# Performance work log

Hardware: AMD Instinct MI355X
Metric: run time of the kernel (lower is better)

The kernel has to match this reference:

```python
import jax, jax.numpy as jnp
from jax import lax
import numpy as np

EPS = 1e-5

def _conv1x1(x, w, b=None):
    # x: [B,C,H,W], w: [O,C]
    y = jnp.einsum('oc,bchw->bohw', w, x)
    if b is not None:
        y = y + b[:, None, None]
    return y

def _bn(x, g, b, m, v):
    scale = g / jnp.sqrt(v + EPS)
    return (x - m[:, None, None]) * scale[:, None, None] + b[:, None, None]

def _conv_bn_silu(x, w, g, b, m, v):
    return jax.nn.silu(_bn(_conv1x1(x, w), g, b, m, v))

def _maxpool(x, k):
    p = k // 2
    return lax.reduce_window(x, -jnp.inf, lax.max, (1, 1, k, k), (1, 1, 1, 1),
                             ((0, 0), (0, 0), (p, p), (p, p)))

def _avgpool(x, k):
    # torch AvgPool2d default count_include_pad=True -> divide by k*k
    p = k // 2
    s = lax.reduce_window(x, 0.0, lax.add, (1, 1, k, k), (1, 1, 1, 1),
                          ((0, 0), (0, 0), (p, p), (p, p)))
    return s / float(k * k)

def setup_inputs() -> dict:
    key = jax.random.key(0)
    ks = jax.random.split(key, 18)
    f32 = jnp.float32
    B, C1, H, W = 8, 512, 64, 64
    c_ = C1 // 2          # 256
    C = c_ * 7            # 1792
    Cq = C // 8           # 224
    C2 = 512
    rn = lambda i, sh, s: jax.random.normal(ks[i], sh, dtype=f32) * s
    return {
        'x': rn(0, (B, C1, H, W), 1.0),
        'cv1_w': rn(1, (c_, C1), 0.05),
        'cv1_g': jax.random.uniform(ks[2], (c_,), dtype=f32),
        'cv1_b': rn(3, (c_,), 0.05),
        'cv1_m': jnp.zeros((c_,), f32),
        'cv1_v': jnp.ones((c_,), f32),
        'q_w': rn(4, (Cq, C), 0.02),
        'q_b': rn(5, (Cq,), 0.02),
        'k_w': rn(6, (Cq, C), 0.02),
        'k_b': rn(7, (Cq,), 0.02),
        'v_w': rn(8, (C, C), 0.02),
        'v_b': rn(9, (C,), 0.02),
        'gamma': rn(10, (1,), 0.5),
        'cv2_w': rn(11, (C2, C), 0.02),
        'cv2_g': jax.random.uniform(ks[12], (C2,), dtype=f32),
        'cv2_b': rn(13, (C2,), 0.05),
        'cv2_m': jnp.zeros((C2,), f32),
        'cv2_v': jnp.ones((C2,), f32),
    }

def _criss_cross(cat, q_w, q_b, k_w, k_b, v_w, v_b, gamma):
    B, C, H, W = cat.shape
    q = _conv1x1(cat, q_w, q_b)   # [B,Cq,H,W]
    k = _conv1x1(cat, k_w, k_b)
    v = _conv1x1(cat, v_w, v_b)   # [B,C,H,W]
    # column (H-axis) energies with -inf diagonal, row (W-axis) energies
    eH = jnp.einsum('bchw,bcgw->bhwg', q, k)        # [B,H,W,H]
    diag = jnp.eye(H, dtype=bool)[:, None, :]       # mask where h == g
    eH = jnp.where(diag, -jnp.inf, eH)
    eW = jnp.einsum('bchw,bchv->bhwv', q, k)        # [B,H,W,W]
    att = jax.nn.softmax(jnp.concatenate([eH, eW], axis=-1), axis=-1)
    attH, attW = att[..., :H], att[..., H:]
    outH = jnp.einsum('bcgw,bhwg->bchw', v, attH)
    outW = jnp.einsum('bchv,bhwv->bchw', v, attW)
    return gamma[0] * (outH + outW) + cat

def reference(x, cv1_w, cv1_g, cv1_b, cv1_m, cv1_v,
              q_w, q_b, k_w, k_b, v_w, v_b, gamma,
              cv2_w, cv2_g, cv2_b, cv2_m, cv2_v):
    x1 = _conv_bn_silu(x, cv1_w, cv1_g, cv1_b, cv1_m, cv1_v)   # [B,256,H,W]
    y1 = _maxpool(x1, 5)
    y2 = _maxpool(y1, 5)
    y3 = _maxpool(y2, 5)
    a1 = _avgpool(x1, 13)
    a2 = _avgpool(x1, 9)
    a3 = _avgpool(x1, 5)
    cat = jnp.concatenate([x1, y1, y2, y3, a1, a2, a3], axis=1)  # [B,1792,H,W]
    att = _criss_cross(cat, q_w, q_b, k_w, k_b, v_w, v_b, gamma)
    return _conv_bn_silu(att, cv2_w, cv2_g, cv2_b, cv2_m, cv2_v)
```

## Files before the change

### kernel.cpp

```cpp
#include <hip/hip_runtime.h>


typedef short bf16x8 __attribute__((ext_vector_type(8)));
typedef float f32x4  __attribute__((ext_vector_type(4)));

#define DEV __device__ __forceinline__

DEV float bf2f(unsigned short u) {
    unsigned int i = ((unsigned int)u) << 16;
    float f; __builtin_memcpy(&f, &i, 4); return f;
}
DEV unsigned short f2bf(float f) {
    unsigned int i; __builtin_memcpy(&i, &f, 4);
    unsigned int r = i + 0x7FFFu + ((i >> 16) & 1u);
    return (unsigned short)(r >> 16);
}
DEV float fsilu(float v) { return v / (1.f + __expf(-v)); }

#define GLL(gsrc, ldst)                                                        \
    __builtin_amdgcn_global_load_lds(                                          \
        (const __attribute__((address_space(1))) unsigned int*)(gsrc),         \
        (__attribute__((address_space(3))) unsigned int*)(ldst), 16, 0, 0)

#define MFMA(a, b, c) __builtin_amdgcn_mfma_f32_16x16x32_bf16((a), (b), (c), 0, 0, 0)

#define SBAR do {                                                              \
    __builtin_amdgcn_sched_barrier(0);                                         \
    __builtin_amdgcn_s_barrier();                                              \
    __builtin_amdgcn_sched_barrier(0); } while (0)
#define LGKM0 do {                                                             \
    asm volatile("s_waitcnt lgkmcnt(0)" ::: "memory");                         \
    __builtin_amdgcn_sched_barrier(0); } while (0)
#define VMC(n) do {                                                            \
    asm volatile("s_waitcnt vmcnt(" #n ")" ::: "memory");                      \
    __builtin_amdgcn_sched_barrier(0); } while (0)

__global__ __launch_bounds__(256) void prep_kernel(
    const float* __restrict__ cv1_w, const float* __restrict__ cv1_g,
    const float* __restrict__ cv1_b, const float* __restrict__ cv1_m,
    const float* __restrict__ cv1_v,
    const float* __restrict__ q_w, const float* __restrict__ q_b,
    const float* __restrict__ k_w, const float* __restrict__ k_b,
    const float* __restrict__ v_b, const float* __restrict__ gamma,
    const float* __restrict__ cv2_w, const float* __restrict__ cv2_g,
    const float* __restrict__ cv2_b, const float* __restrict__ cv2_m,
    const float* __restrict__ cv2_v,
    unsigned short* __restrict__ wb1, unsigned short* __restrict__ wqk,
    unsigned short* __restrict__ wc2,
    float* __restrict__ sc1, float* __restrict__ sh1,
    float* __restrict__ sc2, float* __restrict__ sh2,
    float* __restrict__ qkb, float* __restrict__ zeros)
{
    for (int i = blockIdx.x * 256 + threadIdx.x; i < 917504;
         i += gridDim.x * 256) {
        wc2[i] = f2bf(cv2_w[i]);
        int row = i / 1792;
        int col = i - row * 1792;
        float qv = (row < 224) ? q_w[i]
                   : (row < 448) ? k_w[(row - 224) * 1792 + col] : 0.f;
        wqk[i] = f2bf(qv);
        if (i < 131072) wb1[i] = f2bf(cv1_w[i]);
        if (i < 1792) zeros[i] = 0.f;
        if (i < 512) {
            qkb[i] = (i < 224) ? q_b[i] : (i < 448 ? k_b[i - 224] : 0.f);
            float sc = cv2_g[i] * rsqrtf(cv2_v[i] + 1e-5f);
            float dot = 0.f;
            for (int k = 0; k < 1792; ++k) dot += cv2_w[i * 1792 + k] * v_b[k];
            sc2[i] = sc;
            sh2[i] = cv2_b[i] - cv2_m[i] * sc + sc * gamma[0] * dot;
        }
        if (i < 256) {
            float sc = cv1_g[i] * rsqrtf(cv1_v[i] + 1e-5f);
            sc1[i] = sc; sh1[i] = cv1_b[i] - cv1_m[i] * sc;
        }
    }
}

__global__ __launch_bounds__(256) void transpose_x(
    const float* __restrict__ x, unsigned short* __restrict__ xT)
{
    int bid = blockIdx.x;
    int nt = bid & 63, ct = (bid >> 6) & 7, b = bid >> 9;
    __shared__ float tile[64][65];
    int tid = threadIdx.x;
    int n0 = nt * 64, c0 = ct * 64;
#pragma unroll
    for (int it = 0; it < 16; ++it) {
        int idx = tid + it * 256;
        int r = idx >> 6, cc = idx & 63;
        tile[r][cc] = x[((long)(b * 512 + c0 + r)) * 4096 + n0 + cc];
    }
    __syncthreads();
#pragma unroll
    for (int it = 0; it < 16; ++it) {
        int idx = tid + it * 256;
        int r = idx >> 6, cc = idx & 63;
        xT[((long)(b * 4096 + n0 + r)) * 512 + c0 + cc] = f2bf(tile[cc][r]);
    }
}

__global__ __launch_bounds__(256) void transpose_w(
    const float* __restrict__ w, unsigned short* __restrict__ wT)
{
    int bid = blockIdx.x;
    int tx = bid % 28, ty = bid / 28;
    __shared__ float tile[64][65];
    int tid = threadIdx.x;
#pragma unroll
    for (int it = 0; it < 16; ++it) {
        int idx = tid + it * 256;
        int r = idx >> 6, cc = idx & 63;
        tile[r][cc] = w[((long)(ty * 64 + r)) * 1792 + tx * 64 + cc];
    }
    __syncthreads();
#pragma unroll
    for (int it = 0; it < 16; ++it) {
        int idx = tid + it * 256;
        int r = idx >> 6, cc = idx & 63;
        wT[((long)(tx * 64 + r)) * 1792 + ty * 64 + cc] = f2bf(tile[cc][r]);
    }
}

template <int EPI, bool DUAL>
__global__ __launch_bounds__(512, 2) void gemm256(
    const unsigned short* __restrict__ A, const unsigned short* __restrict__ B,
    const unsigned short* __restrict__ A2, const unsigned short* __restrict__ B2,
    int lda, int ldb, int K1, int K2,
    void* __restrict__ outp, int ldo,
    const float* __restrict__ p0, const float* __restrict__ p1)
{
    __shared__ __align__(16) unsigned short Ash[2][2][8192];
    __shared__ __align__(16) unsigned short Bsh[2][2][8192];
    const int tid = threadIdx.x, lane = tid & 63, wave = tid >> 6;
    const int wm = wave >> 2, wn = wave & 3;
    const long tile_m = (long)blockIdx.x * 256;
    const long tile_n = (long)blockIdx.y * 256;
    const int r0 = tid >> 2;
    const int ke0 = ((tid & 3) * 8) ^ (16 * ((r0 >> 3) & 1));
    const unsigned short* As0 = A + (tile_m + r0) * (long)lda + ke0;
    const unsigned short* As1 = A + (tile_m + r0 + 128) * (long)lda + ke0;
    const unsigned short* Bs0 = B + (tile_n + r0) * (long)ldb + ke0;
    const unsigned short* Bs1 = B + (tile_n + r0 + 128) * (long)ldb + ke0;
    const unsigned short* Cs0 = DUAL ? A2 + (tile_m + r0) * (long)lda + ke0 : As0;
    const unsigned short* Cs1 = DUAL ? A2 + (tile_m + r0 + 128) * (long)lda + ke0 : As1;
    const unsigned short* Ds0 = DUAL ? B2 + (tile_n + r0) * (long)ldb + ke0 : Bs0;
    const unsigned short* Ds1 = DUAL ? B2 + (tile_n + r0 + 128) * (long)ldb + ke0 : Bs1;
    const int dst0 = wave * 512;
    const int dst1 = 4096 + wave * 512;
    const int arow = lane & 15;
    const int kgs = ((lane >> 4) << 3) ^ (16 * ((arow >> 3) & 1));
    f32x4 acc[8][4] = {};
    bf16x8 a[8], b[4];
    const int nt1 = K1 >> 6;
    const int nt = nt1 + (DUAL ? (K2 >> 6) : 0);

#define PA0(t) ((DUAL && (t) >= nt1) ? Cs0 + (long)((t) - nt1) * 64 : As0 + (long)(t) * 64)
#define PA1(t) ((DUAL && (t) >= nt1) ? Cs1 + (long)((t) - nt1) * 64 : As1 + (long)(t) * 64)
#define PB0(t) ((DUAL && (t) >= nt1) ? Ds0 + (long)((t) - nt1) * 64 : Bs0 + (long)(t) * 64)
#define PB1(t) ((DUAL && (t) >= nt1) ? Ds1 + (long)((t) - nt1) * 64 : Bs1 + (long)(t) * 64)
#define STGA(db, kh, t) do {                                                   \
    GLL(PA0(t) + (kh) * 32, &Ash[db][kh][dst0]);                               \
    GLL(PA1(t) + (kh) * 32, &Ash[db][kh][dst1]); } while (0)
#define STGB(db, kh, t) do {                                                   \
    GLL(PB0(t) + (kh) * 32, &Bsh[db][kh][dst0]);                               \
    GLL(PB1(t) + (kh) * 32, &Bsh[db][kh][dst1]); } while (0)
#define LDA8(db, ks) do { _Pragma("unroll")                                    \
    for (int m = 0; m < 8; ++m)                                                \
        a[m] = *(const bf16x8*)&Ash[db][ks][(wm * 128 + m * 16 + arow) * 32 + kgs]; \
    } while (0)
#define LDB1(db, ks, n, slot)                                                  \
    b[slot] = *(const bf16x8*)&Bsh[db][ks][(wn * 64 + (n) * 16 + arow) * 32 + kgs]
#define MMA2(lo) do {                                                          \
    __builtin_amdgcn_s_setprio(1);                                             \
    _Pragma("unroll")                                                          \
    for (int m = 0; m < 8; ++m) {                                              \
        acc[m][lo]     = MFMA(a[m], b[lo],     acc[m][lo]);                    \
        acc[m][lo + 1] = MFMA(a[m], b[lo + 1], acc[m][lo + 1]);                \
    }                                                                          \
    __builtin_amdgcn_s_setprio(0); } while (0)

    STGA(0, 0, 0); STGB(0, 0, 0); STGA(0, 1, 0); STGB(0, 1, 0);
    VMC(4);
    SBAR;

    for (int kt = 0; kt < nt; ++kt) {
        const int db = kt & 1, sb = db ^ 1;
        const bool stg = (kt + 1 < nt);
        const int kn = kt + 1;
        LDA8(db, 0);
        LDB1(db, 0, 0, 0); LDB1(db, 0, 1, 1);
        if (stg) STGA(sb, 0, kn);
        SBAR; LGKM0;
        MMA2(0);
        SBAR;
        LDB1(db, 0, 2, 2); LDB1(db, 0, 3, 3);
        if (stg) STGB(sb, 0, kn);
        SBAR; LGKM0;
        MMA2(2);
        if (kt + 1 < nt) { VMC(4); } else { VMC(0); }
        SBAR;
        LDA8(db, 1);
        LDB1(db, 1, 0, 0); LDB1(db, 1, 1, 1);
        if (stg) STGA(sb, 1, kn);
        SBAR; LGKM0;
        MMA2(0);
        SBAR;
        LDB1(db, 1, 2, 2); LDB1(db, 1, 3, 3);
        if (stg) STGB(sb, 1, kn);
        SBAR; LGKM0;
        MMA2(2);
        if (stg) VMC(4);
        SBAR;
    }

    const int rbase = (lane >> 4) << 2;
#pragma unroll
    for (int n = 0; n < 4; ++n) {
        const int gcol = (int)tile_n + wn * 64 + n * 16 + arow;
        const float s0 = p0[gcol];
        const float s1 = (EPI != 1) ? p1[gcol] : 0.f;
#pragma unroll
        for (int m = 0; m < 8; ++m) {
            const long grow0 = tile_m + wm * 128 + m * 16 + rbase;
            if (EPI == 4) {
                const long bb = grow0 >> 12, pix = grow0 & 4095;
                float4 o4;
#pragma unroll
                for (int r = 0; r < 4; ++r) {
                    float v = acc[m][n][r] * s0 + s1;
                    ((float*)&o4)[r] = fsilu(v);
                }
                *(float4*)&((float*)outp)[((bb * 512 + gcol)) * 4096 + pix] = o4;
            } else {
#pragma unroll
                for (int r = 0; r < 4; ++r) {
                    float v = acc[m][n][r];
                    if (EPI != 1) { v = v * s0 + s1; v = fsilu(v); }
                    else          { v += s0; }
                    ((unsigned short*)outp)[(grow0 + r) * ldo + gcol] = f2bf(v);
                }
            }
        }
    }
#undef PA0
#undef PA1
#undef PB0
#undef PB1
#undef STGA
#undef STGB
#undef LDA8
#undef LDB1
#undef MMA2
}

__global__ __launch_bounds__(256) void pool_h(
    const unsigned short* __restrict__ catT, unsigned short* __restrict__ pool)
{
    const int b = blockIdx.x >> 6, h = blockIdx.x & 63;
    __shared__ __align__(16) unsigned short x1s[64 * 256];
    __shared__ __align__(16) unsigned short rm5[64 * 256];
    const int tid = threadIdx.x, lane = tid & 63, wave = tid >> 6;
    const long nb = (long)b * 4096 + h * 64;
#pragma unroll
    for (int j = 0; j < 8; ++j) {
        int o = wave * 8192 + j * 1024 + lane * 16;
        int w = o >> 9, c = (o & 511) >> 1;
        GLL(catT + (nb + w) * 1792 + c,
            (char*)x1s + (wave * 8192 + j * 1024));
    }
    __syncthreads();
    const int c = tid;
    for (int w = 0; w < 64; ++w) {
        int lo = (w >= 2) ? w - 2 : 0, hi = (w <= 61) ? w + 2 : 63;
        float m = bf2f(x1s[lo * 256 + c]);
        for (int d = lo + 1; d <= hi; ++d) m = fmaxf(m, bf2f(x1s[d * 256 + c]));
        rm5[w * 256 + c] = f2bf(m);
    }
    float s5 = 0.f, s9 = 0.f, s13 = 0.f;
#pragma unroll
    for (int d = 0; d <= 2; ++d) s5  += bf2f(x1s[d * 256 + c]);
#pragma unroll
    for (int d = 0; d <= 4; ++d) s9  += bf2f(x1s[d * 256 + c]);
#pragma unroll
    for (int d = 0; d <= 6; ++d) s13 += bf2f(x1s[d * 256 + c]);
    unsigned short* q0 = pool;
    unsigned short* q1 = pool + (long)32768 * 256;
    unsigned short* q2 = pool + (long)32768 * 512;
    unsigned short* q3 = pool + (long)32768 * 768;
    unsigned short* q4 = pool + (long)32768 * 1024;
    unsigned short* q5 = pool + (long)32768 * 1280;
    const long wb = (long)b * 4096 + h;
    for (int w = 0; w < 64; ++w) {
        long off = (wb + (long)w * 64) * 256 + c;
        float v5 = bf2f(rm5[w * 256 + c]);
        int wm2 = (w >= 2) ? w - 2 : 0, wp2 = (w <= 61) ? w + 2 : 63;
        int wm4 = (w >= 4) ? w - 4 : 0, wp4 = (w <= 59) ? w + 4 : 63;
        float v9  = fmaxf(bf2f(rm5[wm2 * 256 + c]), bf2f(rm5[wp2 * 256 + c]));
        float v13 = fmaxf(v5, fmaxf(bf2f(rm5[wm4 * 256 + c]),
                                    bf2f(rm5[wp4 * 256 + c])));
        q0[off] = f2bf(v5);  q1[off] = f2bf(v9);  q2[off] = f2bf(v13);
        q3[off] = f2bf(s5);  q4[off] = f2bf(s9);  q5[off] = f2bf(s13);
        if (w + 3 <= 63) s5  += bf2f(x1s[(w + 3) * 256 + c]);
        if (w - 2 >= 0)  s5  -= bf2f(x1s[(w - 2) * 256 + c]);
        if (w + 5 <= 63) s9  += bf2f(x1s[(w + 5) * 256 + c]);
        if (w - 4 >= 0)  s9  -= bf2f(x1s[(w - 4) * 256 + c]);
        if (w + 7 <= 63) s13 += bf2f(x1s[(w + 7) * 256 + c]);
        if (w - 6 >= 0)  s13 -= bf2f(x1s[(w - 6) * 256 + c]);
    }
}

template <int I>
__global__ __launch_bounds__(256) void pool_v(
    const unsigned short* __restrict__ pool, unsigned short* __restrict__ catT)
{
    constexpr int R = 2 * (I + 1);
    constexpr int K = 2 * R + 1;
    constexpr float SCL = (I == 0) ? (1.f / 25.f)
                        : (I == 1) ? (1.f / 81.f) : (1.f / 169.f);
    constexpr int MAXD = 256 * (I + 1);
    constexpr int SUMD = 1536 - 256 * I;
    const int bid = blockIdx.x;
    const int chh = bid & 1, w = (bid >> 1) & 63, b = bid >> 7;
    const int c0 = chh * 128;
    __shared__ __align__(16) unsigned short mslab[64 * 128];
    __shared__ __align__(16) unsigned short sslab[64 * 128];
    const int tid = threadIdx.x, lane = tid & 63, wave = tid >> 6;
    const long sbase = ((long)b * 4096 + (long)w * 64) * 256 + c0;
    const unsigned short* msrc = pool + (long)I * 32768 * 256 + sbase;
    const unsigned short* ssrc = pool + (long)(I + 3) * 32768 * 256 + sbase;
#pragma unroll
    for (int j = 0; j < 4; ++j) {
        int o = j * 4096 + wave * 1024 + lane * 16;
        int hh = o >> 8, ce = (o & 255) >> 1;
        GLL(msrc + hh * 256 + ce, (char*)mslab + (j * 4096 + wave * 1024));
        GLL(ssrc + hh * 256 + ce, (char*)sslab + (j * 4096 + wave * 1024));
    }
    __syncthreads();
    const int c = tid & 127, hg = tid >> 7;
    const int h0 = hg * 32;
    const long dbase = ((long)b * 4096 + w) * 1792 + c0 + c;
    float pre[32];
    {
        float run = -1e30f;
        int ph = (h0 + 2 * R - (K - 1)) % K;
#pragma unroll
        for (int t = 0; t < 32 + K - 1; ++t) {
            int p = h0 + R - (K - 1) + t;
            if (ph == 0) run = -1e30f;
            float v = ((unsigned)p < 64u) ? bf2f(mslab[p * 128 + c]) : -1e30f;
            run = fmaxf(run, v);
            if (t >= K - 1) pre[t - (K - 1)] = run;
            ph = (ph + 1 == K) ? 0 : ph + 1;
        }
    }
    {
        float run = -1e30f;
        int ph = (h0 + 31 + (K - 1)) % K;
#pragma unroll
        for (int t = 0; t < 32 + K - 1; ++t) {
            int s = h0 + 31 - R + (K - 1) - t;
            if (ph == K - 1) run = -1e30f;
            float v = ((unsigned)s < 64u) ? bf2f(mslab[s * 128 + c]) : -1e30f;
            run = fmaxf(run, v);
            if (t >= K - 1) {
                int h = s + R;
                catT[dbase + MAXD + (long)h * (64 * 1792)] =
                    f2bf(fmaxf(run, pre[31 + (K - 1) - t]));
            }
            ph = (ph == 0) ? K - 1 : ph - 1;
        }
    }
    {
        float s = 0.f;
        int lo0 = (h0 - R >= 0) ? h0 - R : 0;
        int hi0 = (h0 + R <= 63) ? h0 + R : 63;
        for (int d = lo0; d <= hi0; ++d) s += bf2f(sslab[d * 128 + c]);
        for (int hh = 0; hh < 32; ++hh) {
            int h = h0 + hh;
            catT[dbase + SUMD + (long)h * (64 * 1792)] = f2bf(s * SCL);
            if (h + 1 + R <= 63) s += bf2f(sslab[(h + 1 + R) * 128 + c]);
            if (h - R >= 0)      s -= bf2f(sslab[(h - R) * 128 + c]);
        }
    }
}

__global__ __launch_bounds__(256) void scores_h(
    const unsigned short* __restrict__ qk, float* __restrict__ attHlog)
{
    const int b = blockIdx.x >> 6, w = blockIdx.x & 63;
    __shared__ __align__(16) unsigned short Qs[64 * 232];
    __shared__ __align__(16) unsigned short Ks[64 * 232];
    const int tid = threadIdx.x, lane = tid & 63, wave = tid >> 6;
#pragma unroll
    for (int j = 0; j < 14; ++j) {
        int idx = tid + j * 256;
        int s = idx >= 1792;
        int id2 = idx - s * 1792;
        int row = id2 / 28, cb = id2 - row * 28;
        bf16x8 v = *(const bf16x8*)(qk + ((long)b * 4096 + row * 64 + w) * 512 +
                                    s * 224 + cb * 8);
        *(bf16x8*)((s ? Ks : Qs) + row * 232 + cb * 8) = v;
    }
    __syncthreads();
    const int m0 = wave * 16, arow = lane & 15, kc = (lane >> 4) << 3;
    f32x4 acc[4] = {};
#pragma unroll
    for (int ks = 0; ks < 7; ++ks) {
        bf16x8 af = *(const bf16x8*)(Qs + (m0 + arow) * 232 + ks * 32 + kc);
#pragma unroll
        for (int nf = 0; nf < 4; ++nf) {
            bf16x8 bv = *(const bf16x8*)(Ks + (nf * 16 + arow) * 232 + ks * 32 + kc);
            acc[nf] = MFMA(af, bv, acc[nf]);
        }
    }
    const int rb = (lane >> 4) << 2;
#pragma unroll
    for (int nf = 0; nf < 4; ++nf) {
        int g = nf * 16 + arow;
#pragma unroll
        for (int r = 0; r < 4; ++r) {
            int h = m0 + rb + r;
            float v = acc[nf][r];
            if (g == h) v = -1e30f;
            attHlog[((long)(b * 64 + h) * 64 + w) * 64 + g] = v;
        }
    }
}

__global__ __launch_bounds__(256) void scores_w_softmax(
    const unsigned short* __restrict__ qk, const float* __restrict__ attHlog,
    unsigned short* __restrict__ att)
{
    const int b = blockIdx.x >> 6, h = blockIdx.x & 63;
    __shared__ __align__(16) unsigned short Qs[64 * 232];
    __shared__ __align__(16) unsigned short Ks[64 * 232];
    __shared__ float ews[64 * 65];
    const int tid = threadIdx.x, lane = tid & 63, wave = tid >> 6;
    const long nbase = (long)b * 4096 + h * 64;
#pragma unroll
    for (int j = 0; j < 14; ++j) {
        int idx = tid + j * 256;
        int s = idx >= 1792;
        int id2 = idx - s * 1792;
        int row = id2 / 28, cb = id2 - row * 28;
        bf16x8 v = *(const bf16x8*)(qk + (nbase + row) * 512 + s * 224 + cb * 8);
        *(bf16x8*)((s ? Ks : Qs) + row * 232 + cb * 8) = v;
    }
    __syncthreads();
    const int m0 = wave * 16, arow = lane & 15, kc = (lane >> 4) << 3;
    f32x4 acc[4] = {};
#pragma unroll
    for (int ks = 0; ks < 7; ++ks) {
        bf16x8 af = *(const bf16x8*)(Qs + (m0 + arow) * 232 + ks * 32 + kc);
#pragma unroll
        for (int nf = 0; nf < 4; ++nf) {
            bf16x8 bv = *(const bf16x8*)(Ks + (nf * 16 + arow) * 232 + ks * 32 + kc);
            acc[nf] = MFMA(af, bv, acc[nf]);
        }
    }
    const int rb = (lane >> 4) << 2;
#pragma unroll
    for (int nf = 0; nf < 4; ++nf)
#pragma unroll
        for (int r = 0; r < 4; ++r)
            ews[(m0 + rb + r) * 65 + nf * 16 + arow] = acc[nf][r];
    __syncthreads();
    const int wl = tid >> 2, p = tid & 3;
    float eh[16], ew[16];
    const float* hrow = attHlog + ((long)(b * 64 + h) * 64 + wl) * 64 + p * 16;
#pragma unroll
    for (int j = 0; j < 16; ++j) eh[j] = hrow[j];
#pragma unroll
    for (int j = 0; j < 16; ++j) ew[j] = ews[wl * 65 + p * 16 + j];
    float mx = -1e30f;
#pragma unroll
    for (int j = 0; j < 16; ++j) { mx = fmaxf(mx, eh[j]); mx = fmaxf(mx, ew[j]); }
    mx = fmaxf(mx, __shfl_xor(mx, 1));
    mx = fmaxf(mx, __shfl_xor(mx, 2));
    float sm = 0.f;
#pragma unroll
    for (int j = 0; j < 16; ++j) {
        eh[j] = __expf(eh[j] - mx); sm += eh[j];
        ew[j] = __expf(ew[j] - mx); sm += ew[j];
    }
    sm += __shfl_xor(sm, 1);
    sm += __shfl_xor(sm, 2);
    float inv = 1.f / sm;
    unsigned short* orow = att + ((long)(b * 64 + h) * 64 + wl) * 128;
#pragma unroll
    for (int j = 0; j < 16; ++j) orow[p * 16 + j] = f2bf(eh[j] * inv);
#pragma unroll
    for (int j = 0; j < 16; ++j) orow[64 + p * 16 + j] = f2bf(ew[j] * inv);
}

template <int MODE>
__global__ __launch_bounds__(256) void apply_att(
    const unsigned short* __restrict__ att, const unsigned short* __restrict__ vsrc,
    unsigned short* __restrict__ mixed, const float* __restrict__ gamma)
{
    const int ch = blockIdx.x & 3;
    const int i  = (blockIdx.x >> 2) & 63;
    const int b  = blockIdx.x >> 8;
    const int c0 = ch * 448;
    __shared__ __align__(16) unsigned short As[64 * 72];
    __shared__ __align__(16) unsigned short Vs[64 * 448];
    const int tid = threadIdx.x, lane = tid & 63, wave = tid >> 6;
#pragma unroll
    for (int j = 0; j < 2; ++j) {
        int idx = tid + j * 256;
        int hh = idx >> 3, cb = idx & 7;
        long pos = (MODE == 0) ? ((long)(b * 64 + hh) * 64 + i)
                               : ((long)(b * 64 + i) * 64 + hh);
        bf16x8 v = *(const bf16x8*)(att + pos * 128 + MODE * 64 + cb * 8);
        *(bf16x8*)(As + hh * 72 + cb * 8) = v;
    }
#pragma unroll
    for (int j = 0; j < 14; ++j) {
        int idx = tid + j * 256;
        int g = idx / 56, cb = idx - g * 56;
        long n = (MODE == 0) ? ((long)b * 4096 + g * 64 + i)
                             : ((long)b * 4096 + i * 64 + g);
        bf16x8 v = *(const bf16x8*)(vsrc + n * 1792 + c0 + cb * 8);
        int sw = (g >> 3) & 7;
        *(bf16x8*)(Vs + g * 448 + ((cb ^ sw) << 3)) = v;
    }
    __syncthreads();
    const int arow = lane & 15, kc8 = (lane >> 4) << 3;
    const int rb = (lane >> 4) << 2;
    f32x4 acc[4][7] = {};
#pragma unroll
    for (int ks = 0; ks < 2; ++ks) {
        const int k0 = ks * 32;
        bf16x8 af[4];
#pragma unroll
        for (int m = 0; m < 4; ++m)
            af[m] = *(const bf16x8*)(As + (m * 16 + arow) * 72 + k0 + kc8);
        const int g0 = k0 + kc8;
        const int sw = (g0 >> 3) & 7;
#pragma unroll
        for (int nf = 0; nf < 7; ++nf) {
            int cl = wave * 112 + nf * 16 + arow;
            int cb = cl >> 3, clo = cl & 7;
            const unsigned short* pp = Vs + g0 * 448 + ((cb ^ sw) << 3) + clo;
            bf16x8 bv;
#pragma unroll
            for (int j = 0; j < 8; ++j) bv[j] = (short)pp[j * 448];
#pragma unroll
            for (int m = 0; m < 4; ++m)
                acc[m][nf] = MFMA(af[m], bv, acc[m][nf]);
        }
    }
    const float gam = gamma[0];
#pragma unroll
    for (int nf = 0; nf < 7; ++nf) {
        const int c = c0 + wave * 112 + nf * 16 + arow;
#pragma unroll
        for (int m = 0; m < 4; ++m) {
#pragma unroll
            for (int r = 0; r < 4; ++r) {
                const int rl = m * 16 + rb + r;
                long n = (MODE == 0) ? ((long)b * 4096 + rl * 64 + i)
                                     : ((long)b * 4096 + i * 64 + rl);
                long idx2 = n * 1792 + c;
                if (MODE == 0) {
                    mixed[idx2] = f2bf(acc[m][nf][r]);
                } else {
                    float pv = bf2f(mixed[idx2]);
                    mixed[idx2] = f2bf(gam * (acc[m][nf][r] + pv));
                }
            }
        }
    }
}

extern "C" void kernel_launch(void* const* d_in, const int* in_sizes, int n_in,
                              void* d_out, int out_size, void* d_ws, size_t ws_size,
                              hipStream_t stream)
{
    const float* x     = (const float*)d_in[0];
    const float* cv1_w = (const float*)d_in[1];
    const float* cv1_g = (const float*)d_in[2];
    const float* cv1_b = (const float*)d_in[3];
    const float* cv1_m = (const float*)d_in[4];
    const float* cv1_v = (const float*)d_in[5];
    const float* q_w   = (const float*)d_in[6];
    const float* q_b   = (const float*)d_in[7];
    const float* k_w   = (const float*)d_in[8];
    const float* k_b   = (const float*)d_in[9];
    const float* v_w   = (const float*)d_in[10];
    const float* v_b   = (const float*)d_in[11];
    const float* gamma = (const float*)d_in[12];
    const float* cv2_w = (const float*)d_in[13];
    const float* cv2_g = (const float*)d_in[14];
    const float* cv2_b = (const float*)d_in[15];
    const float* cv2_m = (const float*)d_in[16];
    const float* cv2_v = (const float*)d_in[17];

    char* ws = (char*)d_ws;
    unsigned short* wb1  = (unsigned short*)(ws + 0);
    unsigned short* wqk  = (unsigned short*)(ws + 262144);
    unsigned short* wc2  = (unsigned short*)(ws + 2097152);
    unsigned short* w2g  = (unsigned short*)(ws + 3932160);
    float* sc1           = (float*)(ws + 5767168);
    float* sh1           = (float*)(ws + 5775360);
    float* sc2           = (float*)(ws + 5783552);
    float* sh2           = (float*)(ws + 5791744);
    float* qkb           = (float*)(ws + 5799936);
    float* zeros         = (float*)(ws + 5808128);
    unsigned short* catT = (unsigned short*)(ws + 6291456);
    const long C_OFF = 123731968;
    unsigned short* xT    = (unsigned short*)(ws + C_OFF);
    unsigned short* wvT   = (unsigned short*)(ws + C_OFF + 33554432);
    unsigned short* poolb = (unsigned short*)(ws + C_OFF);
    unsigned short* mixed = (unsigned short*)(ws + C_OFF);
    unsigned short* qk    = (unsigned short*)d_out;
    float* attHlog        = (float*)((char*)d_out + 33554432);
    unsigned short* attb  = (unsigned short*)((char*)d_out + 41943040);

    prep_kernel<<<1024, 256, 0, stream>>>(
        cv1_w, cv1_g, cv1_b, cv1_m, cv1_v, q_w, q_b, k_w, k_b, v_b, gamma,
        cv2_w, cv2_g, cv2_b, cv2_m, cv2_v,
        wb1, wqk, wc2, sc1, sh1, sc2, sh2, qkb, zeros);

    transpose_x<<<4096, 256, 0, stream>>>(x, xT);
    transpose_w<<<784, 256, 0, stream>>>(v_w, wvT);

    gemm256<1, false><<<dim3(2, 7), 512, 0, stream>>>(
        wc2, wvT, wc2, wvT, 1792, 1792, 1792, 0, w2g, 1792, zeros, nullptr);

    gemm256<0, false><<<dim3(128, 1), 512, 0, stream>>>(
        xT, wb1, xT, wb1, 512, 512, 512, 0, catT, 1792, sc1, sh1);

    pool_h<<<512, 256, 0, stream>>>(catT, poolb);
    pool_v<0><<<1024, 256, 0, stream>>>(poolb, catT);
    pool_v<1><<<1024, 256, 0, stream>>>(poolb, catT);
    pool_v<2><<<1024, 256, 0, stream>>>(poolb, catT);

    gemm256<1, false><<<dim3(128, 2), 512, 0, stream>>>(
        catT, wqk, catT, wqk, 1792, 1792, 1792, 0, qk, 512, qkb, nullptr);

    scores_h<<<512, 256, 0, stream>>>(qk, attHlog);
    scores_w_softmax<<<512, 256, 0, stream>>>(qk, attHlog, attb);

    apply_att<0><<<2048, 256, 0, stream>>>(attb, catT, mixed, gamma);
    apply_att<1><<<2048, 256, 0, stream>>>(attb, catT, mixed, gamma);

    gemm256<4, true><<<dim3(128, 2), 512, 0, stream>>>(
        mixed, w2g, catT, wc2, 1792, 1792, 1792, 1792, d_out, 0, sc2, sh2);
}
```

Before: 640.1 us.

## Deepen GEMM LDS prefetch pipeline and split horizontal pooling per kernel size

```diff
diff --git a/kernel.cpp b/kernel.cpp
--- a/kernel.cpp
+++ b/kernel.cpp
@@ -179,37 +179,42 @@
     }                                                                          \
     __builtin_amdgcn_s_setprio(0); } while (0)
 
-    STGA(0, 0, 0); STGB(0, 0, 0); STGA(0, 1, 0); STGB(0, 1, 0);
-    VMC(4);
+    STGA(0, 0, 0); STGB(0, 0, 0);
+    STGA(0, 1, 0); STGB(0, 1, 0);
+    {
+        const int t1p = (1 < nt) ? 1 : 0;
+        STGA(1, 0, t1p); STGB(1, 0, t1p);
+    }
+    VMC(8);
     SBAR;
 
     for (int kt = 0; kt < nt; ++kt) {
         const int db = kt & 1, sb = db ^ 1;
-        const bool stg = (kt + 1 < nt);
-        const int kn = kt + 1;
+        const int t1c = (kt + 1 < nt) ? kt + 1 : nt - 1;
+        const int t2c = (kt + 2 < nt) ? kt + 2 : nt - 1;
         LDA8(db, 0);
         LDB1(db, 0, 0, 0); LDB1(db, 0, 1, 1);
-        if (stg) STGA(sb, 0, kn);
+        STGA(sb, 1, t1c);
         SBAR; LGKM0;
         MMA2(0);
         SBAR;
         LDB1(db, 0, 2, 2); LDB1(db, 0, 3, 3);
-        if (stg) STGB(sb, 0, kn);
+        STGB(sb, 1, t1c);
         SBAR; LGKM0;
         MMA2(2);
-        if (kt + 1 < nt) { VMC(4); } else { VMC(0); }
+        VMC(8);
         SBAR;
         LDA8(db, 1);
         LDB1(db, 1, 0, 0); LDB1(db, 1, 1, 1);
-        if (stg) STGA(sb, 1, kn);
+        STGA(db, 0, t2c);
         SBAR; LGKM0;
         MMA2(0);
         SBAR;
         LDB1(db, 1, 2, 2); LDB1(db, 1, 3, 3);
-        if (stg) STGB(sb, 1, kn);
+        STGB(db, 0, t2c);
         SBAR; LGKM0;
         MMA2(2);
-        if (stg) VMC(4);
+        VMC(8);
         SBAR;
     }
 
@@ -253,59 +258,71 @@
 #undef MMA2
 }
 
-__global__ __launch_bounds__(256) void pool_h(
+template <int I>
+__global__ __launch_bounds__(512) void pool_hk(
     const unsigned short* __restrict__ catT, unsigned short* __restrict__ pool)
 {
+    constexpr int R = 2 * (I + 1);
+    constexpr int K = 2 * R + 1;
     const int b = blockIdx.x >> 6, h = blockIdx.x & 63;
     __shared__ __align__(16) unsigned short x1s[64 * 256];
-    __shared__ __align__(16) unsigned short rm5[64 * 256];
     const int tid = threadIdx.x, lane = tid & 63, wave = tid >> 6;
     const long nb = (long)b * 4096 + h * 64;
 #pragma unroll
-    for (int j = 0; j < 8; ++j) {
-        int o = wave * 8192 + j * 1024 + lane * 16;
-        int w = o >> 9, c = (o & 511) >> 1;
-        GLL(catT + (nb + w) * 1792 + c,
-            (char*)x1s + (wave * 8192 + j * 1024));
-    }
-    __syncthreads();
-    const int c = tid;
-    for (int w = 0; w < 64; ++w) {
-        int lo = (w >= 2) ? w - 2 : 0, hi = (w <= 61) ? w + 2 : 63;
-        float m = bf2f(x1s[lo * 256 + c]);
-        for (int d = lo + 1; d <= hi; ++d) m = fmaxf(m, bf2f(x1s[d * 256 + c]));
-        rm5[w * 256 + c] = f2bf(m);
-    }
-    float s5 = 0.f, s9 = 0.f, s13 = 0.f;
-#pragma unroll
-    for (int d = 0; d <= 2; ++d) s5  += bf2f(x1s[d * 256 + c]);
-#pragma unroll
-    for (int d = 0; d <= 4; ++d) s9  += bf2f(x1s[d * 256 + c]);
-#pragma unroll
-    for (int d = 0; d <= 6; ++d) s13 += bf2f(x1s[d * 256 + c]);
-    unsigned short* q0 = pool;
-    unsigned short* q1 = pool + (long)32768 * 256;
-    unsigned short* q2 = pool + (long)32768 * 512;
-    unsigned short* q3 = pool + (long)32768 * 768;
-    unsigned short* q4 = pool + (long)32768 * 1024;
-    unsigned short* q5 = pool + (long)32768 * 1280;
-    const long wb = (long)b * 4096 + h;
-    for (int w = 0; w < 64; ++w) {
-        long off = (wb + (long)w * 64) * 256 + c;
-        float v5 = bf2f(rm5[w * 256 + c]);
-        int wm2 = (w >= 2) ? w - 2 : 0, wp2 = (w <= 61) ? w + 2 : 63;
-        int wm4 = (w >= 4) ? w - 4 : 0, wp4 = (w <= 59) ? w + 4 : 63;
-        float v9  = fmaxf(bf2f(rm5[wm2 * 256 + c]), bf2f(rm5[wp2 * 256 + c]));
-        float v13 = fmaxf(v5, fmaxf(bf2f(rm5[wm4 * 256 + c]),
-                                    bf2f(rm5[wp4 * 256 + c])));
-        q0[off] = f2bf(v5);  q1[off] = f2bf(v9);  q2[off] = f2bf(v13);
-        q3[off] = f2bf(s5);  q4[off] = f2bf(s9);  q5[off] = f2bf(s13);
-        if (w + 3 <= 63) s5  += bf2f(x1s[(w + 3) * 256 + c]);
-        if (w - 2 >= 0)  s5  -= bf2f(x1s[(w - 2) * 256 + c]);
-        if (w + 5 <= 63) s9  += bf2f(x1s[(w + 5) * 256 + c]);
-        if (w - 4 >= 0)  s9  -= bf2f(x1s[(w - 4) * 256 + c]);
-        if (w + 7 <= 63) s13 += bf2f(x1s[(w + 7) * 256 + c]);
-        if (w - 6 >= 0)  s13 -= bf2f(x1s[(w - 6) * 256 + c]);
+    for (int j = 0; j < 4; ++j) {
+        int chunk = j * 8 + wave;
+        int o = chunk * 1024 + lane * 16;
+        int e = o >> 1, w = e >> 8, c = e & 255;
+        GLL(catT + (nb + w) * 1792 + c, (char*)x1s + chunk * 1024);
+    }
+    __syncthreads();
+    const int c = tid & 255, wg = tid >> 8;
+    const int w0 = wg * 32;
+    unsigned short* qm = pool + (long)I * 32768 * 256;
+    unsigned short* qs = pool + (long)(I + 3) * 32768 * 256;
+    const long obase = ((long)b * 4096 + h) * 256 + c;
+    float pre[32];
+    {
+        float run = -1e30f;
+        int ph = (w0 + 2 * R - (K - 1)) % K;
+#pragma unroll
+        for (int t = 0; t < 32 + K - 1; ++t) {
+            int p = w0 + R - (K - 1) + t;
+            if (ph == 0) run = -1e30f;
+            float v = ((unsigned)p < 64u) ? bf2f(x1s[p * 256 + c]) : -1e30f;
+            run = fmaxf(run, v);
+            if (t >= K - 1) pre[t - (K - 1)] = run;
+            ph = (ph + 1 == K) ? 0 : ph + 1;
+        }
+    }
+    {
+        float run = -1e30f;
+        int ph = (w0 + 31 + (K - 1)) % K;
+#pragma unroll
+        for (int t = 0; t < 32 + K - 1; ++t) {
+            int s = w0 + 31 - R + (K - 1) - t;
+            if (ph == K - 1) run = -1e30f;
+            float v = ((unsigned)s < 64u) ? bf2f(x1s[s * 256 + c]) : -1e30f;
+            run = fmaxf(run, v);
+            if (t >= K - 1) {
+                int w = s + R;
+                qm[obase + (long)w * 16384] =
+                    f2bf(fmaxf(run, pre[31 + (K - 1) - t]));
+            }
+            ph = (ph == 0) ? K - 1 : ph - 1;
+        }
+    }
+    {
+        float s = 0.f;
+        int lo0 = (w0 - R >= 0) ? w0 - R : 0;
+        int hi0 = (w0 + R <= 63) ? w0 + R : 63;
+        for (int d = lo0; d <= hi0; ++d) s += bf2f(x1s[d * 256 + c]);
+        for (int ww = 0; ww < 32; ++ww) {
+            int w = w0 + ww;
+            qs[obase + (long)w * 16384] = f2bf(s);
+            if (w + 1 + R <= 63) s += bf2f(x1s[(w + 1 + R) * 256 + c]);
+            if (w - R >= 0)      s -= bf2f(x1s[(w - R) * 256 + c]);
+        }
     }
 }
 
@@ -631,7 +648,9 @@
     gemm256<0, false><<<dim3(128, 1), 512, 0, stream>>>(
         xT, wb1, xT, wb1, 512, 512, 512, 0, catT, 1792, sc1, sh1);
 
-    pool_h<<<512, 256, 0, stream>>>(catT, poolb);
+    pool_hk<0><<<512, 512, 0, stream>>>(catT, poolb);
+    pool_hk<1><<<512, 512, 0, stream>>>(catT, poolb);
+    pool_hk<2><<<512, 512, 0, stream>>>(catT, poolb);
     pool_v<0><<<1024, 256, 0, stream>>>(poolb, catT);
     pool_v<1><<<1024, 256, 0, stream>>>(poolb, catT);
     pool_v<2><<<1024, 256, 0, stream>>>(poolb, catT);
```

Result: no change. 634.3 us (-0.9%).
